# Optimization experiments

Hardware: AMD Instinct MI355X
Metric: run time of the kernel (lower is better)

The kernel has to match this reference:

```python
import jax, jax.numpy as jnp
import numpy as np

B, T, D, H, L, OUT, FC = 256, 512, 64, 256, 2, 1, 128


def setup_inputs() -> dict:
    key = jax.random.key(0)
    ks = jax.random.split(key, 16)
    s = 1.0 / np.sqrt(H)
    u = lambda k, shape: jax.random.uniform(k, shape, jnp.float32, -s, s)
    return {
        "x": jax.random.normal(ks[0], (B, T, D), jnp.float32),
        # layer 0 LSTM params (PyTorch gate order: i, f, g, o)
        "W_ih0": u(ks[1], (4 * H, D)),
        "W_hh0": u(ks[2], (4 * H, H)),
        "b_ih0": u(ks[3], (4 * H,)),
        "b_hh0": u(ks[4], (4 * H,)),
        # layer 1 LSTM params
        "W_ih1": u(ks[5], (4 * H, H)),
        "W_hh1": u(ks[6], (4 * H, H)),
        "b_ih1": u(ks[7], (4 * H,)),
        "b_hh1": u(ks[8], (4 * H,)),
        # MLP head
        "fc1_w": u(ks[9], (FC, H)),
        "fc1_b": u(ks[10], (FC,)),
        "fc2_w": u(ks[11], (OUT, FC)),
        "fc2_b": u(ks[12], (OUT,)),
    }


def _lstm_layer(x, W_ih, W_hh, b_ih, b_hh):
    # x: [B, T, Din] -> (outputs [B, T, H], final hidden [B, H])
    Bsz = x.shape[0]
    Hh = W_hh.shape[1]
    # precompute input contribution to all gates: [B, T, 4H]
    xg = jnp.einsum("btd,gd->btg", x, W_ih) + b_ih + b_hh

    def step(carry, xt):
        h, c = carry
        g = xt + h @ W_hh.T  # [B, 4H]
        i, f, gg, o = jnp.split(g, 4, axis=-1)
        i = jax.nn.sigmoid(i)
        f = jax.nn.sigmoid(f)
        gg = jnp.tanh(gg)
        o = jax.nn.sigmoid(o)
        c = f * c + i * gg
        h = o * jnp.tanh(c)
        return (h, c), h

    h0 = jnp.zeros((Bsz, Hh), x.dtype)
    (hT, _cT), hs = jax.lax.scan(step, (h0, h0), jnp.swapaxes(xg, 0, 1))
    return jnp.swapaxes(hs, 0, 1), hT


def reference(x, W_ih0, W_hh0, b_ih0, b_hh0, W_ih1, W_hh1, b_ih1, b_hh1,
              fc1_w, fc1_b, fc2_w, fc2_b):
    # eval-mode forward: inter-layer dropout (p=0.2) is a no-op
    y0, h0f = _lstm_layer(x, W_ih0, W_hh0, b_ih0, b_hh0)
    _y1, h1f = _lstm_layer(y0, W_ih1, W_hh1, b_ih1, b_hh1)
    # h_n.view(-1, H): stack per-layer final hidden states -> [L*B, H]
    h_n = jnp.concatenate([h0f, h1f], axis=0)
    out = jax.nn.relu(h_n)
    out = jax.nn.relu(out @ fc1_w.T + fc1_b)
    return out @ fc2_w.T + fc2_b  # [L*B, OUT]
```

## Files before the change

kernel.cpp:

```cpp
#include <hip/hip_runtime.h>

#define Bb 256
#define Tt 512
#define Dd 64
#define Hh 256
#define NP 16
#define HB2 (256 * 256)
#define FSTRIDE 16

typedef unsigned short u16;
typedef _Float16 f16;
typedef __attribute__((ext_vector_type(8))) _Float16 f16x8;
typedef __attribute__((ext_vector_type(4))) _Float16 f16x4;
typedef __attribute__((ext_vector_type(4))) float f32x4;
typedef __attribute__((ext_vector_type(4))) unsigned int u32x4;

__device__ __forceinline__ f16x8 bc8h(u32x4 v) { return __builtin_bit_cast(f16x8, v); }

__device__ __forceinline__ float fsig(float x) {
  x = fminf(fmaxf(x, -30.f), 30.f);
  return 1.f / (1.f + __expf(-x));
}
__device__ __forceinline__ float ftanh(float x) {
  x = fminf(fmaxf(x, -15.f), 15.f);
  float t = __expf(2.f * x);
  return (t - 1.f) / (t + 1.f);
}

__device__ __forceinline__ f16x8 ld16_sc1(const f16* p) {
  f16x8 r;
  asm volatile("global_load_dwordx4 %0, %1, off sc1" : "=v"(r) : "v"(p) : "memory");
  return r;
}
__device__ __forceinline__ f16x8 ld16_sc0(const f16* p) {
  f16x8 r;
  asm volatile("global_load_dwordx4 %0, %1, off sc0" : "=v"(r) : "v"(p) : "memory");
  return r;
}
__device__ __forceinline__ void st2_sc1(f16* p, unsigned v) {
  asm volatile("global_store_short %0, %1, off sc1" : : "v"(p), "v"(v) : "memory");
}
__device__ __forceinline__ void st2_plain(f16* p, unsigned v) {
  asm volatile("global_store_short %0, %1, off" : : "v"(p), "v"(v) : "memory");
}
__device__ __forceinline__ void st4u_plain(unsigned* p, unsigned v) {
  asm volatile("global_store_dword %0, %1, off" : : "v"(p), "v"(v) : "memory");
}
__device__ __forceinline__ void st4u_sc1(unsigned* p, unsigned v) {
  asm volatile("global_store_dword %0, %1, off sc1" : : "v"(p), "v"(v) : "memory");
}
__device__ __forceinline__ unsigned ld4_sc0(const unsigned* p) {
  unsigned r;
  asm volatile("global_load_dword %0, %1, off sc0\n\ts_waitcnt vmcnt(0)"
               : "=v"(r) : "v"(p) : "memory");
  return r;
}
__device__ __forceinline__ void atomswap_l2(unsigned* p, unsigned v) {
  asm volatile("global_atomic_swap %0, %1, off" : : "v"(p), "v"(v) : "memory");
}
__device__ __forceinline__ unsigned atomadd0_l2(unsigned* p) {
  unsigned r;
  asm volatile("global_atomic_add %0, %1, %2, off sc0\n\ts_waitcnt vmcnt(0)"
               : "=v"(r) : "v"(p), "v"(0u) : "memory");
  return r;
}

__global__ __launch_bounds__(256) void prep_x(const float* __restrict__ x,
                                              f16* __restrict__ xh) {
  int i = blockIdx.x * blockDim.x + threadIdx.x;
  const int n4 = Bb * Tt * Dd / 4;
  if (i >= n4) return;
  f32x4 v = ((const f32x4*)x)[i];
  f16x4 o;
#pragma unroll
  for (int j = 0; j < 4; ++j) o[j] = (f16)v[j];
  ((f16x4*)xh)[i] = o;
}

__global__ __launch_bounds__(256) void prep_w(
    const float* __restrict__ wih0, const float* __restrict__ whh0,
    const float* __restrict__ bih0, const float* __restrict__ bhh0,
    const float* __restrict__ wih1, const float* __restrict__ whh1,
    const float* __restrict__ bih1, const float* __restrict__ bhh1,
    f16* __restrict__ wfrag, float* __restrict__ bias0s, float* __restrict__ bias1s) {
  int tid = blockIdx.x * blockDim.x + threadIdx.x;
  int np = gridDim.x * blockDim.x;
  const int tot = 16 * 8 * 32 * 512;
  for (int u = tid; u < tot; u += np) {
    int e = u & 7, l = (u >> 3) & 63;
    int f = (u >> 9) & 31;
    int wv = (u >> 14) & 7;
    int p = u >> 17;
    int g = wv & 3;
    int grow = g * 256 + p * 16 + (l & 15);
    int klane = (l >> 4) * 8 + e;
    float w = 0.f;
    if (wv < 4) {
      if (f < 4)       w = wih0[grow * 64 + (f >> 1) * 32 + klane];
      else if (f < 20) w = whh0[grow * 256 + ((f - 4) >> 1) * 32 + klane];
    } else {
      if (f < 16)      w = wih1[grow * 256 + (f >> 1) * 32 + klane];
      else             w = whh1[grow * 256 + ((f - 16) >> 1) * 32 + klane];
    }
    f16 hi = (f16)w;
    wfrag[u] = (f & 1) ? (f16)((w - (float)hi) * 2048.0f) : hi;
  }
  for (int u = tid; u < 1024; u += np) {
    bias0s[u] = bih0[u] + bhh0[u];
    bias1s[u] = bih1[u] + bhh1[u];
  }
}

#define MF(A, B, C) __builtin_amdgcn_mfma_f32_16x16x32_f16(A, B, C, 0, 0, 0)

__global__ __launch_bounds__(512, 2) void lstm_persist(
    const f16* __restrict__ xh, const f16* __restrict__ wfrag,
    const float* __restrict__ bias0s, const float* __restrict__ bias1s,
    f16* h0, f16* h1, unsigned* flags, unsigned* flagsL2, unsigned* probe,
    unsigned* verdict) {
  const int bid = blockIdx.x;
  const int p = (bid >> 3) & 15;
  const int grp = (bid & 7) * 2 + (bid >> 7);
  const int tid = threadIdx.x;
  const int wv = tid >> 6, lane = tid & 63;
  const int lr = lane & 15, lk = lane >> 4;
  const int g = wv & 3;
  const bool isL1 = wv >= 4;
  const float LOSCALE = 1.0f / 2048.0f;

  __shared__ float gbuf[2][4][16][16];
  __shared__ u32x4 hbuf[2][16][36];
  __shared__ unsigned s_fast;

  f16x8 wf[32];
  {
    const u32x4* wp = (const u32x4*)wfrag + ((size_t)(p * 8 + wv) * 32) * 64 + lane;
#pragma unroll
    for (int f = 0; f < 20; ++f) wf[f] = bc8h(wp[(size_t)f * 64]);
    if (isL1) {
#pragma unroll
      for (int f = 20; f < 32; ++f) wf[f] = bc8h(wp[(size_t)f * 64]);
    }
  }
  const float bias = (isL1 ? bias1s : bias0s)[g * 256 + p * 16 + lr];

  if (tid < 256) {
    int lsel = tid >> 7;
    int d = tid & 127;
    int row = d >> 3, cp = d & 7;
    f16* base = lsel ? h1 : (h0 + (size_t)3 * HB2);
    unsigned* w = (unsigned*)(base + (size_t)(grp * 16 + row) * 256 + p * 16) + cp;
    st4u_plain(w, 0u);
    st4u_sc1(w, 0u);
  }
  if (tid == 0) atomswap_l2(&flagsL2[(grp * NP + p) * FSTRIDE], 0u);
  asm volatile("s_waitcnt vmcnt(0)" ::: "memory");
  __syncthreads();

  if (wv == 0) {
    if (lane == 0) {
      st4u_plain(&probe[grp * NP + p], (unsigned)(p + 1));
      asm volatile("s_waitcnt vmcnt(0)" ::: "memory");
    }
    bool seen = (lane >= NP);
    bool ok;
    int it = 0;
    while (true) {
      if (!seen) {
        unsigned got = ld4_sc0(&probe[grp * NP + lane]);
        if (got == (unsigned)(lane + 1)) seen = true;
      }
      if (__all(seen)) { ok = true; break; }
      if (++it > 768) { ok = false; break; }
      __builtin_amdgcn_s_sleep(2);
    }
    if (lane == 0)
      __hip_atomic_store(&verdict[grp * NP + p], ok ? 1u : 2u, __ATOMIC_RELAXED,
                         __HIP_MEMORY_SCOPE_AGENT);
    unsigned v;
    while (true) {
      v = 1u;
      if (lane < NP)
        v = __hip_atomic_load(&verdict[grp * NP + lane], __ATOMIC_RELAXED,
                              __HIP_MEMORY_SCOPE_AGENT);
      if (!__any(v == 0u)) break;
      __builtin_amdgcn_s_sleep(2);
    }
    if (lane == 0) s_fast = __any(v != 1u) ? 0u : 1u;
  }
  __syncthreads();
  const bool fast = (s_fast != 0u);

  const int eL = tid >> 8;
  const int erow = (tid >> 4) & 15, ecol = tid & 15;
  float c = 0.f;
  f16* const hout = ((eL ? h1 : h0) + (size_t)(grp * 16 + erow) * 256 + p * 16 + ecol);

  const int hrow = grp * 16 + lr;
  const f16* xbase = xh + (size_t)hrow * Tt * Dd + lk * 8;
  const f16* hsrcbase = ((wv < 4) ? h0 : h1) + (size_t)grp * 4096;
  const int hlsel = wv >> 2;

  for (int k = 0; k <= Tt; ++k) {
    f32x4 a = (f32x4){bias, bias, bias, bias};
    f32x4 b = (f32x4){0.f, 0.f, 0.f, 0.f};
    if (!isL1 && k < Tt) {
      const u32x4* xp = (const u32x4*)(xbase + (size_t)k * Dd);
      f16x8 xf0 = bc8h(xp[0]);
      f16x8 xf1 = bc8h(xp[4]);
      a = MF(xf0, wf[0], a);
      b = MF(xf0, wf[1], b);
      a = MF(xf1, wf[2], a);
      b = MF(xf1, wf[3], b);
    }

    if (wv == 0) {
      int spin = 0;
      bool ready = false;
      while (!ready) {
        unsigned v = 0xFFFFFFFFu;
        if (lane < NP) {
          if (fast) {
            v = atomadd0_l2(&flagsL2[(grp * NP + lane) * FSTRIDE]);
            if ((++spin & 63) == 0) {
              unsigned v3 = __hip_atomic_load(&flags[(grp * NP + lane) * FSTRIDE],
                                              __ATOMIC_RELAXED,
                                              __HIP_MEMORY_SCOPE_AGENT);
              if (v3 > v) v = v3;
            }
          } else {
            v = __hip_atomic_load(&flags[(grp * NP + lane) * FSTRIDE],
                                  __ATOMIC_RELAXED, __HIP_MEMORY_SCOPE_AGENT);
          }
        }
        ready = !__any(v < (unsigned)k);
        if (!ready) __builtin_amdgcn_s_sleep(1);
      }
    }
    asm volatile("" ::: "memory");
    __syncthreads();

    const int par = (k - 1) & 3;

    {
      const f16* src = hsrcbase + (size_t)par * HB2;
      const int j0 = (wv & 3) * 2;
      const f16* p0 = src + j0 * 512 + lane * 8;
      f16x8 s0, s1;
      if (fast) {
        s0 = ld16_sc0(p0);
        s1 = ld16_sc0(p0 + 512);
      } else {
        s0 = ld16_sc1(p0);
        s1 = ld16_sc1(p0 + 512);
      }
      asm volatile("s_waitcnt vmcnt(0)" ::: "memory");
      const int r0 = j0 * 2 + (lane >> 5);
      const int c2 = lane & 31;
      hbuf[hlsel][r0][c2 ^ (r0 & 7)] = __builtin_bit_cast(u32x4, s0);
      hbuf[hlsel][r0 + 2][c2 ^ ((r0 + 2) & 7)] = __builtin_bit_cast(u32x4, s1);
    }
    __syncthreads();

    f16x8 A0[8], A1[8];
#pragma unroll
    for (int kt = 0; kt < 8; ++kt)
      A0[kt] = __builtin_bit_cast(f16x8, hbuf[0][lr][(kt * 4 + lk) ^ (lr & 7)]);
    if (isL1) {
#pragma unroll
      for (int kt = 0; kt < 8; ++kt)
        A1[kt] = __builtin_bit_cast(f16x8, hbuf[1][lr][(kt * 4 + lk) ^ (lr & 7)]);
    }

    if (!isL1) {
      if (k < Tt) {
#pragma unroll
        for (int kt = 0; kt < 8; ++kt) {
          a = MF(A0[kt], wf[4 + 2 * kt], a);
          b = MF(A0[kt], wf[5 + 2 * kt], b);
        }
        a += b * LOSCALE;
#pragma unroll
        for (int r = 0; r < 4; ++r) gbuf[0][g][lk * 4 + r][lr] = a[r];
      }
    } else if (k >= 1) {
#pragma unroll
      for (int kt = 0; kt < 8; ++kt) {
        a = MF(A0[kt], wf[2 * kt], a);
        b = MF(A0[kt], wf[2 * kt + 1], b);
      }
#pragma unroll
      for (int kt = 0; kt < 8; ++kt) {
        a = MF(A1[kt], wf[16 + 2 * kt], a);
        b = MF(A1[kt], wf[17 + 2 * kt], b);
      }
      a += b * LOSCALE;
#pragma unroll
      for (int r = 0; r < 4; ++r) gbuf[1][g][lk * 4 + r][lr] = a[r];
    }
    __syncthreads();

    {
      const bool upd = eL ? (k >= 1) : (k < Tt);
      if (upd) {
        float iv = fsig(gbuf[eL][0][erow][ecol]);
        float fv = fsig(gbuf[eL][1][erow][ecol]);
        float gv = ftanh(gbuf[eL][2][erow][ecol]);
        float ov = fsig(gbuf[eL][3][erow][ecol]);
        c = fv * c + iv * gv;
        float hval = ov * ftanh(c);
        f16 fh = (f16)hval;
        unsigned bits = (unsigned)__builtin_bit_cast(u16, fh);
        f16* Ho = hout + (size_t)(k & 3) * HB2;
        if (fast) st2_plain(Ho, bits);
        else      st2_sc1(Ho, bits);
      }
    }
    asm volatile("s_waitcnt vmcnt(0)" ::: "memory");
    __syncthreads();
    if (tid == 0) {
      unsigned nv = (unsigned)(k + 1);
      if (fast) atomswap_l2(&flagsL2[(grp * NP + p) * FSTRIDE], nv);
      __hip_atomic_store(&flags[(grp * NP + p) * FSTRIDE], nv, __ATOMIC_RELAXED,
                         __HIP_MEMORY_SCOPE_AGENT);
    }
  }
}

__global__ __launch_bounds__(128) void head_kernel(
    const f16* __restrict__ h0f, const f16* __restrict__ h1f,
    const float* __restrict__ fc1w, const float* __restrict__ fc1b,
    const float* __restrict__ fc2w, const float* __restrict__ fc2b,
    float* __restrict__ out) {
  int r = blockIdx.x;
  const f16* hh = (r < 256) ? (h0f + r * Hh) : (h1f + (r - 256) * Hh);
  __shared__ float v[Hh];
  int tid = threadIdx.x;
  for (int i = tid; i < Hh; i += 128)
    v[i] = fmaxf((float)hh[i], 0.f);
  __syncthreads();
  float s = fc1b[tid];
#pragma unroll 8
  for (int i = 0; i < Hh; ++i) s += fc1w[tid * Hh + i] * v[i];
  s = fmaxf(s, 0.f) * fc2w[tid];
#pragma unroll
  for (int off = 32; off; off >>= 1) s += __shfl_down(s, off);
  __shared__ float red[2];
  if ((tid & 63) == 0) red[tid >> 6] = s;
  __syncthreads();
  if (tid == 0) out[r] = red[0] + red[1] + fc2b[0];
}

extern "C" void kernel_launch(void* const* d_in, const int* in_sizes, int n_in,
                              void* d_out, int out_size, void* d_ws, size_t ws_size,
                              hipStream_t stream) {
  (void)in_sizes; (void)n_in; (void)out_size; (void)ws_size;
  const float* x    = (const float*)d_in[0];
  const float* wih0 = (const float*)d_in[1];
  const float* whh0 = (const float*)d_in[2];
  const float* bih0 = (const float*)d_in[3];
  const float* bhh0 = (const float*)d_in[4];
  const float* wih1 = (const float*)d_in[5];
  const float* whh1 = (const float*)d_in[6];
  const float* bih1 = (const float*)d_in[7];
  const float* bhh1 = (const float*)d_in[8];
  const float* fc1w = (const float*)d_in[9];
  const float* fc1b = (const float*)d_in[10];
  const float* fc2w = (const float*)d_in[11];
  const float* fc2b = (const float*)d_in[12];

  char* ws = (char*)d_ws;
  size_t off = 0;
  f16* xh = (f16*)(ws + off); off += (size_t)Bb * Tt * Dd * 2;
  f16* wfrag = (f16*)(ws + off); off += (size_t)16 * 8 * 32 * 512 * 2;
  float* bias0s = (float*)(ws + off); off += 4096;
  float* bias1s = (float*)(ws + off); off += 4096;
  char* zbase = ws + off;
  f16* h0 = (f16*)(ws + off); off += (size_t)4 * HB2 * 2;
  f16* h1 = (f16*)(ws + off); off += (size_t)4 * HB2 * 2;
  unsigned* flags = (unsigned*)(ws + off); off += 256 * FSTRIDE * 4;
  unsigned* flagsL2 = (unsigned*)(ws + off); off += 256 * FSTRIDE * 4;
  unsigned* probe = (unsigned*)(ws + off); off += 1024;
  unsigned* verdict = (unsigned*)(ws + off); off += 1024;
  size_t zbytes = (size_t)((ws + off) - zbase);

  hipMemsetAsync(zbase, 0, zbytes, stream);
  prep_x<<<Bb * Tt * Dd / 4 / 256, 256, 0, stream>>>(x, xh);
  prep_w<<<512, 256, 0, stream>>>(wih0, whh0, bih0, bhh0, wih1, whh1, bih1, bhh1,
                                  wfrag, bias0s, bias1s);
  lstm_persist<<<256, 512, 0, stream>>>(xh, wfrag, bias0s, bias1s, h0, h1, flags,
                                        flagsL2, probe, verdict);
  head_kernel<<<512, 128, 0, stream>>>(h0 + (size_t)3 * HB2, h1, fc1w, fc1b,
                                       fc2w, fc2b, (float*)d_out);
}
```

Baseline: 1.507 ms.

## Replace block barriers and flag swaps with per-wave counter increments and LDS mailbox

Removes the two __syncthreads per timestep. Each wave now atomically increments a per-block counter after its stores, and consumers wait until the counter reaches 8*k. Only wave 0 polls the remote counters; the other waves spin on an LDS mailbox instead of a block barrier. The two flag arrays are merged into one, and launch bounds change from 2 to 1 blocks per CU. The spin loop gains a timeout break, and the removed barriers create possible intra-block ordering hazards on the shared gbuf/hbuf buffers.

```diff
diff --git a/kernel.cpp b/kernel.cpp
--- a/kernel.cpp
+++ b/kernel.cpp
@@ -57,6 +57,9 @@
 }
 __device__ __forceinline__ void atomswap_l2(unsigned* p, unsigned v) {
   asm volatile("global_atomic_swap %0, %1, off" : : "v"(p), "v"(v) : "memory");
+}
+__device__ __forceinline__ void atomadd_l2(unsigned* p, unsigned v) {
+  asm volatile("global_atomic_add %0, %1, off" : : "v"(p), "v"(v) : "memory");
 }
 __device__ __forceinline__ unsigned atomadd0_l2(unsigned* p) {
   unsigned r;
@@ -113,11 +116,10 @@
 
 #define MF(A, B, C) __builtin_amdgcn_mfma_f32_16x16x32_f16(A, B, C, 0, 0, 0)
 
-__global__ __launch_bounds__(512, 2) void lstm_persist(
+__global__ __launch_bounds__(512, 1) void lstm_persist(
     const f16* __restrict__ xh, const f16* __restrict__ wfrag,
     const float* __restrict__ bias0s, const float* __restrict__ bias1s,
-    f16* h0, f16* h1, unsigned* flags, unsigned* flagsL2, unsigned* probe,
-    unsigned* verdict) {
+    f16* h0, f16* h1, unsigned* flagcnt, unsigned* probe, unsigned* verdict) {
   const int bid = blockIdx.x;
   const int p = (bid >> 3) & 15;
   const int grp = (bid & 7) * 2 + (bid >> 7);
@@ -131,6 +133,9 @@
   __shared__ float gbuf[2][4][16][16];
   __shared__ u32x4 hbuf[2][16][36];
   __shared__ unsigned s_fast;
+  __shared__ int s_mbox;
+
+  if (tid == 0) s_mbox = -1;
 
   f16x8 wf[32];
   {
@@ -153,7 +158,11 @@
     st4u_plain(w, 0u);
     st4u_sc1(w, 0u);
   }
-  if (tid == 0) atomswap_l2(&flagsL2[(grp * NP + p) * FSTRIDE], 0u);
+  if (tid == 0) {
+    atomswap_l2(&flagcnt[(grp * NP + p) * FSTRIDE], 0u);
+    __hip_atomic_store(&flagcnt[(grp * NP + p) * FSTRIDE], 0u, __ATOMIC_RELAXED,
+                       __HIP_MEMORY_SCOPE_AGENT);
+  }
   asm volatile("s_waitcnt vmcnt(0)" ::: "memory");
   __syncthreads();
 
@@ -200,6 +209,7 @@
   const f16* xbase = xh + (size_t)hrow * Tt * Dd + lk * 8;
   const f16* hsrcbase = ((wv < 4) ? h0 : h1) + (size_t)grp * 4096;
   const int hlsel = wv >> 2;
+  unsigned* const mycnt = &flagcnt[(grp * NP + p) * FSTRIDE];
 
   for (int k = 0; k <= Tt; ++k) {
     f32x4 a = (f32x4){bias, bias, bias, bias};
@@ -215,30 +225,32 @@
     }
 
     if (wv == 0) {
-      int spin = 0;
+      const unsigned thr = 8u * (unsigned)k;
+      int it = 0;
       bool ready = false;
       while (!ready) {
         unsigned v = 0xFFFFFFFFu;
         if (lane < NP) {
-          if (fast) {
-            v = atomadd0_l2(&flagsL2[(grp * NP + lane) * FSTRIDE]);
-            if ((++spin & 63) == 0) {
-              unsigned v3 = __hip_atomic_load(&flags[(grp * NP + lane) * FSTRIDE],
-                                              __ATOMIC_RELAXED,
-                                              __HIP_MEMORY_SCOPE_AGENT);
-              if (v3 > v) v = v3;
-            }
-          } else {
-            v = __hip_atomic_load(&flags[(grp * NP + lane) * FSTRIDE],
+          if (fast)
+            v = atomadd0_l2(&flagcnt[(grp * NP + lane) * FSTRIDE]);
+          else
+            v = __hip_atomic_load(&flagcnt[(grp * NP + lane) * FSTRIDE],
                                   __ATOMIC_RELAXED, __HIP_MEMORY_SCOPE_AGENT);
-          }
         }
-        ready = !__any(v < (unsigned)k);
-        if (!ready) __builtin_amdgcn_s_sleep(1);
-      }
+        ready = !__any(v < thr);
+        if (!ready) {
+          if (++it > 65536) break;
+          __builtin_amdgcn_s_sleep(1);
+        }
+      }
+      __hip_atomic_store(&s_mbox, k, __ATOMIC_RELAXED,
+                         __HIP_MEMORY_SCOPE_WORKGROUP);
+    } else {
+      while (__hip_atomic_load(&s_mbox, __ATOMIC_RELAXED,
+                               __HIP_MEMORY_SCOPE_WORKGROUP) < k)
+        __builtin_amdgcn_s_sleep(1);
     }
     asm volatile("" ::: "memory");
-    __syncthreads();
 
     const int par = (k - 1) & 3;
 
@@ -317,12 +329,10 @@
       }
     }
     asm volatile("s_waitcnt vmcnt(0)" ::: "memory");
-    __syncthreads();
-    if (tid == 0) {
-      unsigned nv = (unsigned)(k + 1);
-      if (fast) atomswap_l2(&flagsL2[(grp * NP + p) * FSTRIDE], nv);
-      __hip_atomic_store(&flags[(grp * NP + p) * FSTRIDE], nv, __ATOMIC_RELAXED,
-                         __HIP_MEMORY_SCOPE_AGENT);
+    if (lane == 0) {
+      if (fast) atomadd_l2(mycnt, 1u);
+      else (void)__hip_atomic_fetch_add(mycnt, 1u, __ATOMIC_RELAXED,
+                                        __HIP_MEMORY_SCOPE_AGENT);
     }
   }
 }
@@ -378,8 +388,7 @@
   char* zbase = ws + off;
   f16* h0 = (f16*)(ws + off); off += (size_t)4 * HB2 * 2;
   f16* h1 = (f16*)(ws + off); off += (size_t)4 * HB2 * 2;
-  unsigned* flags = (unsigned*)(ws + off); off += 256 * FSTRIDE * 4;
-  unsigned* flagsL2 = (unsigned*)(ws + off); off += 256 * FSTRIDE * 4;
+  unsigned* flagcnt = (unsigned*)(ws + off); off += 256 * FSTRIDE * 4;
   unsigned* probe = (unsigned*)(ws + off); off += 1024;
   unsigned* verdict = (unsigned*)(ws + off); off += 1024;
   size_t zbytes = (size_t)((ws + off) - zbase);
@@ -388,8 +397,8 @@
   prep_x<<<Bb * Tt * Dd / 4 / 256, 256, 0, stream>>>(x, xh);
   prep_w<<<512, 256, 0, stream>>>(wih0, whh0, bih0, bhh0, wih1, whh1, bih1, bhh1,
                                   wfrag, bias0s, bias1s);
-  lstm_persist<<<256, 512, 0, stream>>>(xh, wfrag, bias0s, bias1s, h0, h1, flags,
-                                        flagsL2, probe, verdict);
+  lstm_persist<<<256, 512, 0, stream>>>(xh, wfrag, bias0s, bias1s, h0, h1,
+                                        flagcnt, probe, verdict);
   head_kernel<<<512, 128, 0, stream>>>(h0 + (size_t)3 * HB2, h1, fc1w, fc1b,
                                        fc2w, fc2b, (float*)d_out);
 }
```

Measured after the change: 1.425 ms. 5.5% less time.
